# Optimization experiments

Measured on AMD Instinct MI355X. Metric: run time of the kernel, lower is better.

The kernel has to match this reference:

```python
import jax, jax.numpy as jnp
import numpy as np

B, C, U, V, H, W = 4, 64, 5, 5, 64, 64
MID = 64  # mid_dim defaults to dim


def setup_inputs() -> dict:
    key = jax.random.key(0)
    ks = jax.random.split(key, 13)
    s = 0.05
    inp = {"x": jax.random.normal(ks[0], (B, C, U, V, H, W), dtype=jnp.float32)}
    # body: Conv2d(dim->mid,1x1), SiLU, Conv2d(mid->dim,1x1)
    inp["w1"] = jax.random.normal(ks[1], (MID, C), dtype=jnp.float32) * s
    inp["b1"] = jax.random.normal(ks[2], (MID,), dtype=jnp.float32) * s
    inp["w2"] = jax.random.normal(ks[3], (C, MID), dtype=jnp.float32) * s
    inp["b2"] = jax.random.normal(ks[4], (C,), dtype=jnp.float32) * s
    # four fuse 1x1 convs (dim->dim)
    for i in range(4):
        inp[f"fw{i}"] = jax.random.normal(ks[5 + 2 * i], (C, C), dtype=jnp.float32) * s
        inp[f"fb{i}"] = jax.random.normal(ks[6 + 2 * i], (C,), dtype=jnp.float32) * s
    return inp


def _conv1x1(w, b, x):
    # x: (B,C,h,w); w: (O,C); 1x1 conv == channel matmul
    return jnp.einsum('oc,bchw->bohw', w, x) + b[None, :, None, None]


def reference(x, w1, b1, w2, b2, fw0, fb0, fw1, fb1, fw2, fb2, fw3, fb3):
    # Four 2-axis mean pools over the 6D tensor
    hw_m = x.mean(axis=(2, 3))   # (B,C,H,W)
    uv_m = x.mean(axis=(4, 5))   # (B,C,U,V)
    uh_m = x.mean(axis=(3, 5))   # (B,C,U,H)
    vw_m = x.mean(axis=(2, 4))   # (B,C,V,W)
    # Assemble padded buffer uvhw of shape (B,C,H+V,W+U)
    top = jnp.concatenate([hw_m, jnp.swapaxes(uh_m, -1, -2)], axis=-1)  # (B,C,H,W+U)
    bot = jnp.concatenate([vw_m, jnp.swapaxes(uv_m, -1, -2)], axis=-1)  # (B,C,V,W+U)
    uvhw = jnpp_concat = jnp.concatenate([top, bot], axis=-2)           # (B,C,H+V,W+U)
    # body: conv1x1 -> SiLU -> conv1x1
    uvhw = _conv1x1(w2, b2, jax.nn.silu(_conv1x1(w1, b1, uvhw)))
    # Split back into the four pooled maps
    hw = uvhw[..., :H, :W]
    vw = uvhw[..., H:, :W]
    uh = jnp.swapaxes(uvhw[..., :H, W:], -1, -2)  # (B,C,U,H)
    uv = jnp.swapaxes(uvhw[..., H:, W:], -1, -2)  # (B,C,U,V)
    # Per-branch fuse convs, then broadcast-gate x and sum
    hw = _conv1x1(fw0, fb0, hw).reshape(B, C, 1, 1, H, W)
    uv = _conv1x1(fw1, fb1, uv).reshape(B, C, U, V, 1, 1)
    uh = _conv1x1(fw2, fb2, uh).reshape(B, C, U, 1, H, 1)
    vw = _conv1x1(fw3, fb3, vw).reshape(B, C, 1, V, 1, W)
    return x * hw + x * uv + x * uh + x * vw
```

## Files before the change

### kernel.cpp

```cpp
#include <hip/hip_runtime.h>
#include <hip/hip_bf16.h>
#include <cstddef>

#define BB 4
#define CC 64
#define UU 5
#define VV 5
#define HH 64
#define WW 64

typedef float f4v __attribute__((ext_vector_type(4)));

__device__ __forceinline__ float rdlane(float v, int l) {
    return __uint_as_float((unsigned)__builtin_amdgcn_readlane((int)__float_as_uint(v), l));
}
__device__ __forceinline__ float rfl(float v) {
    return __uint_as_float((unsigned)__builtin_amdgcn_readfirstlane((int)__float_as_uint(v)));
}
__device__ __forceinline__ float sum4(float4 a) { return (a.x+a.y)+(a.z+a.w); }
__device__ __forceinline__ void nt_store4(float4 r, float4* p) {
    union { float4 s; f4v v; } u; u.s = r;
    __builtin_nontemporal_store(u.v, (f4v*)p);
}

__global__ __launch_bounds__(1024) void k1_means(const float* __restrict__ x,
        float* __restrict__ m_hw, float* __restrict__ R,
        float* __restrict__ vw_part) {
    const int bc   = blockIdx.x;
    const int t    = threadIdx.x;
    const int wave = t >> 6;
    const int lane = t & 63;

    const float4* xt = (const float4*)x + (size_t)bc * 25600;

    __shared__ float smem[25*1024];

    float4 hw = make_float4(0.f,0.f,0.f,0.f);
    float4 vwacc[5];
    #pragma unroll
    for (int v = 0; v < 5; ++v) vwacc[v] = make_float4(0.f,0.f,0.f,0.f);

    #pragma unroll
    for (int k = 0; k < 25; ++k) {
        float4 q = xt[(size_t)k*1024 + t];
        hw.x += q.x; hw.y += q.y; hw.z += q.z; hw.w += q.w;
        const int v = k % 5;
        vwacc[v].x += q.x; vwacc[v].y += q.y;
        vwacc[v].z += q.z; vwacc[v].w += q.w;
        smem[k*1024 + t] = sum4(q);
    }

    float4 o;
    o.x = hw.x*(1.f/25.f); o.y = hw.y*(1.f/25.f);
    o.z = hw.z*(1.f/25.f); o.w = hw.w*(1.f/25.f);
    ((float4*)m_hw)[(size_t)bc*1024 + t] = o;

    __syncthreads();

    for (int task = t; task < 1600; task += 1024) {
        const int k = task >> 6, h = task & 63;
        const float* row = &smem[k*1024 + h*16];
        float s = 0.f;
        #pragma unroll
        for (int j = 0; j < 16; ++j) s += row[j];
        R[((size_t)bc*25 + k)*64 + h] = s;
    }
    __syncthreads();

    float4* vwbuf = (float4*)smem;
    #pragma unroll
    for (int v = 0; v < 5; ++v) {
        float4 s = vwacc[v];
        s.x += __shfl_xor(s.x, 16); s.y += __shfl_xor(s.y, 16);
        s.z += __shfl_xor(s.z, 16); s.w += __shfl_xor(s.w, 16);
        s.x += __shfl_xor(s.x, 32); s.y += __shfl_xor(s.y, 32);
        s.z += __shfl_xor(s.z, 32); s.w += __shfl_xor(s.w, 32);
        if (lane < 16) vwbuf[(wave*5 + v)*16 + lane] = s;
    }
    __syncthreads();

    if (t < 80) {
        const int v = t >> 4;
        float4 s = vwbuf[(0*5 + v)*16 + (t & 15)];
        #pragma unroll
        for (int w16 = 1; w16 < 16; ++w16) {
            float4 pp = vwbuf[(w16*5 + v)*16 + (t & 15)];
            s.x += pp.x; s.y += pp.y; s.z += pp.z; s.w += pp.w;
        }
        ((float4*)vw_part)[(size_t)bc*80 + t] = s;
    }
}

#define LOADROW(dst, src)                                              \
    { _Pragma("unroll")                                                \
      for (int q = 0; q < 16; ++q) {                                   \
          float4 t4 = ((const float4*)(src))[lane*16 + q];             \
          dst[4*q+0] = t4.x; dst[4*q+1] = t4.y;                        \
          dst[4*q+2] = t4.z; dst[4*q+3] = t4.w;                        \
      } }

#define DOT64(res, wr, src)                                            \
    float res;                                                         \
    { float _a0=0.f,_a1=0.f,_a2=0.f,_a3=0.f;                           \
      _Pragma("unroll")                                                \
      for (int cc2 = 0; cc2 < 64; cc2 += 4) {                          \
          _a0 = fmaf(wr[cc2+0], rdlane(src, cc2+0), _a0);              \
          _a1 = fmaf(wr[cc2+1], rdlane(src, cc2+1), _a1);              \
          _a2 = fmaf(wr[cc2+2], rdlane(src, cc2+2), _a2);              \
          _a3 = fmaf(wr[cc2+3], rdlane(src, cc2+3), _a3);              \
      }                                                                \
      res = (_a0 + _a1) + (_a2 + _a3); }

#define MLP_CORE(VIN, OUTEXPR)                                         \
    {                                                                  \
        float v = (VIN);                                               \
        DOT64(d1, w1r, v);                                             \
        float acc1 = d1 + b1v;                                         \
        float ya = acc1 / (1.f + __expf(-acc1));                       \
        DOT64(d2, w2r, ya);                                            \
        float acc2 = d2 + b2v;                                         \
        DOT64(d3, fr, acc2);                                           \
        OUTEXPR = d3 + fbv;                                            \
    }

__global__ __launch_bounds__(64, 1) void k2_mlp(
        const float* __restrict__ m_hw, const float* __restrict__ R,
        const float* __restrict__ vw_part,
        const float* __restrict__ w1, const float* __restrict__ b1,
        const float* __restrict__ w2, const float* __restrict__ b2,
        const float* __restrict__ fw0, const float* __restrict__ fb0,
        const float* __restrict__ fw1, const float* __restrict__ fb1,
        const float* __restrict__ fw2, const float* __restrict__ fb2,
        const float* __restrict__ fw3, const float* __restrict__ fb3,
        float* __restrict__ mod_hw, float* __restrict__ mod_uh,
        float* __restrict__ mod_vw, float* __restrict__ mod_uv) {
    const int blk  = blockIdx.x;
    const int row  = blk / 3;
    const int chnk = blk % 3;
    const int b    = row / 69;
    const int i    = row % 69;
    const int lane = threadIdx.x & 63;

    const int j0 = chnk * 23;
    const int j1 = min(69, j0 + 23);
    const bool top = (i < 64);

    const float* fwA = top ? fw0 : fw3;
    const float* fbA = top ? fb0 : fb3;
    const float* fwB = top ? fw2 : fw1;
    const float* fbB = top ? fb2 : fb1;

    float w1r[64], w2r[64], fr[64];
    LOADROW(w1r, w1);
    LOADROW(w2r, w2);
    const float b1v = b1[lane];
    const float b2v = b2[lane];

    const int b64c = b * CC + lane;
    const int cbl  = b64c;

    const int jm = min(j1, 64);
    if (j0 < jm) {
        LOADROW(fr, fwA);
        const float fbv = fbA[lane];
        if (top) {
            const float* src = m_hw + (size_t)b64c*4096 + i*64;
            float* sp = mod_hw + ((size_t)cbl*64 + i)*64;
            for (int j = j0; j < jm; ++j)
                MLP_CORE(src[j], sp[j])
        } else {
            const float* pv = vw_part + (size_t)b64c*320 + (i-64)*64;
            float* sp = mod_vw + (size_t)cbl*320 + (i-64)*64;
            for (int j = j0; j < jm; ++j)
                MLP_CORE(pv[j] * (1.f/320.f), sp[j])
        }
    }
    if (j1 > 64) {
        LOADROW(fr, fwB);
        const float fbv = fbB[lane];
        const int jb = max(j0, 64);
        if (top) {
            float* sp = mod_uh + (size_t)cbl*320 + i;
            for (int j = jb; j < j1; ++j) {
                const int u = j - 64;
                const float* Rp = R + ((size_t)b64c*25 + u*5)*64 + i;
                float vin = (Rp[0] + Rp[64] + Rp[128] + Rp[192] + Rp[256])
                            * (1.f/320.f);
                MLP_CORE(vin, sp[(size_t)u*64])
            }
        } else {
            float* sp = mod_uv + (size_t)cbl*25 + (i-64);
            for (int j = jb; j < j1; ++j) {
                const int u = j - 64;
                const float4* Rp4 = (const float4*)(R
                    + ((size_t)b64c*25 + u*5 + (i-64))*64);
                float4 a = make_float4(0.f,0.f,0.f,0.f);
                #pragma unroll
                for (int k = 0; k < 16; ++k) {
                    float4 pp = Rp4[k];
                    a.x += pp.x; a.y += pp.y; a.z += pp.z; a.w += pp.w;
                }
                MLP_CORE(sum4(a) * (1.f/4096.f), sp[(size_t)u*5])
            }
        }
    }
}

__global__ __launch_bounds__(256, 4) void k3_apply(
        const float* __restrict__ x,
        const float* __restrict__ mod_hw, const float* __restrict__ mod_uh,
        const float* __restrict__ mod_vw, const float* __restrict__ mod_uv,
        float* __restrict__ out) {
    const int blk  = blockIdx.x;
    const int bc   = blk >> 2;
    const int qt   = blk & 3;
    const int t    = threadIdx.x;
    const int base = qt*256 + t;
    const int h    = base >> 4;

    float4 mh = ((const float4*)(mod_hw + (size_t)bc * 4096))[base];
    float uh[5];
    #pragma unroll
    for (int u = 0; u < 5; ++u) uh[u] = mod_uh[(size_t)bc*320 + u*64 + h];
    float4 vw[5];
    #pragma unroll
    for (int v = 0; v < 5; ++v)
        vw[v] = ((const float4*)(mod_vw + (size_t)bc*320 + v*64))[t & 15];
    float uv[25];
    #pragma unroll
    for (int k = 0; k < 25; ++k)
        uv[k] = rfl(mod_uv[(size_t)bc*25 + k]);

    const float4* x4 = (const float4*)(x + (size_t)bc * (UU*VV*HH*WW));
    float4* o4 = (float4*)(out + (size_t)bc * (UU*VV*HH*WW));

    #pragma unroll
    for (int u = 0; u < 5; ++u) {
        #pragma unroll
        for (int v = 0; v < 5; ++v) {
            const int idx = (u*5 + v)*1024 + base;
            float4 xv = x4[idx];
            const float s = uh[u] + uv[u*5 + v];
            float4 r;
            r.x = xv.x * (mh.x + vw[v].x + s);
            r.y = xv.y * (mh.y + vw[v].y + s);
            r.z = xv.z * (mh.z + vw[v].z + s);
            r.w = xv.w * (mh.w + vw[v].w + s);
            nt_store4(r, &o4[idx]);
        }
    }
}

extern "C" void kernel_launch(void* const* d_in, const int* in_sizes, int n_in,
                              void* d_out, int out_size, void* d_ws, size_t ws_size,
                              hipStream_t stream) {
    const float* x   = (const float*)d_in[0];
    const float* w1  = (const float*)d_in[1];
    const float* b1  = (const float*)d_in[2];
    const float* w2  = (const float*)d_in[3];
    const float* b2  = (const float*)d_in[4];
    const float* fw0 = (const float*)d_in[5];
    const float* fb0 = (const float*)d_in[6];
    const float* fw1 = (const float*)d_in[7];
    const float* fb1 = (const float*)d_in[8];
    const float* fw2 = (const float*)d_in[9];
    const float* fb2 = (const float*)d_in[10];
    const float* fw3 = (const float*)d_in[11];
    const float* fb3 = (const float*)d_in[12];

    float* ws = (float*)d_ws;
    float* mod_hw = ws;
    float* mod_uh = mod_hw + 1048576;
    float* mod_vw = mod_uh + 81920;
    float* mod_uv = mod_vw + 81920;

    float* m_hw    = (float*)d_out;
    float* Rbuf    = m_hw + 1048576;
    float* vw_part = Rbuf + 409600;

    k1_means<<<BB*CC, 1024, 0, stream>>>(x, m_hw, Rbuf, vw_part);
    k2_mlp<<<BB*69*3, 64, 0, stream>>>(m_hw, Rbuf, vw_part, w1, b1, w2, b2,
                                       fw0, fb0, fw1, fb1, fw2, fb2, fw3, fb3,
                                       mod_hw, mod_uh, mod_vw, mod_uv);
    k3_apply<<<BB*CC*4, 256, 0, stream>>>(x, mod_hw, mod_uh, mod_vw, mod_uv,
                                          (float*)d_out);
}
```

Measured before the change: 90.99 us.

## Split means kernel into four 256-thread blocks per channel with register-batched loads

The pooling kernel now launches four 256-thread blocks per (b,c) slice instead of one 1024-thread block, each covering a quarter of the H rows. All 25 float4 loads are issued up front into registers, and shared memory shrinks fourfold, which should improve occupancy and memory-level parallelism. The vw partial sums are now written per quarter-block, and the MLP kernel reduces the four partials itself, adding a few extra loads there.

```diff
diff --git a/kernel.cpp b/kernel.cpp
--- a/kernel.cpp
+++ b/kernel.cpp
@@ -23,47 +23,54 @@
     __builtin_nontemporal_store(u.v, (f4v*)p);
 }
 
-__global__ __launch_bounds__(1024) void k1_means(const float* __restrict__ x,
+__global__ __launch_bounds__(256) void k1_means(const float* __restrict__ x,
         float* __restrict__ m_hw, float* __restrict__ R,
         float* __restrict__ vw_part) {
-    const int bc   = blockIdx.x;
+    const int bid = blockIdx.x;
+    const int bc  = bid >> 2;
+    const int qt  = bid & 3;
     const int t    = threadIdx.x;
+    const int p    = qt*256 + t;
     const int wave = t >> 6;
     const int lane = t & 63;
 
-    const float4* xt = (const float4*)x + (size_t)bc * 25600;
-
-    __shared__ float smem[25*1024];
+    const float4* xt = (const float4*)x + (size_t)bc * 25600 + p;
+
+    __shared__ float smem[25*256];
+
+    float4 q[25];
+    #pragma unroll
+    for (int k = 0; k < 25; ++k)
+        q[k] = xt[(size_t)k*1024];
 
     float4 hw = make_float4(0.f,0.f,0.f,0.f);
     float4 vwacc[5];
     #pragma unroll
     for (int v = 0; v < 5; ++v) vwacc[v] = make_float4(0.f,0.f,0.f,0.f);
-
     #pragma unroll
     for (int k = 0; k < 25; ++k) {
-        float4 q = xt[(size_t)k*1024 + t];
-        hw.x += q.x; hw.y += q.y; hw.z += q.z; hw.w += q.w;
+        hw.x += q[k].x; hw.y += q[k].y; hw.z += q[k].z; hw.w += q[k].w;
         const int v = k % 5;
-        vwacc[v].x += q.x; vwacc[v].y += q.y;
-        vwacc[v].z += q.z; vwacc[v].w += q.w;
-        smem[k*1024 + t] = sum4(q);
+        vwacc[v].x += q[k].x; vwacc[v].y += q[k].y;
+        vwacc[v].z += q[k].z; vwacc[v].w += q[k].w;
+        smem[k*256 + t] = sum4(q[k]);
     }
 
     float4 o;
     o.x = hw.x*(1.f/25.f); o.y = hw.y*(1.f/25.f);
     o.z = hw.z*(1.f/25.f); o.w = hw.w*(1.f/25.f);
-    ((float4*)m_hw)[(size_t)bc*1024 + t] = o;
+    ((float4*)m_hw)[(size_t)bc*1024 + p] = o;
 
     __syncthreads();
 
-    for (int task = t; task < 1600; task += 1024) {
-        const int k = task >> 6, h = task & 63;
-        const float* row = &smem[k*1024 + h*16];
+    for (int task = t; task < 400; task += 256) {
+        const int k    = task >> 4;
+        const int hloc = task & 15;
+        const float* row = &smem[k*256 + hloc*16];
         float s = 0.f;
         #pragma unroll
         for (int j = 0; j < 16; ++j) s += row[j];
-        R[((size_t)bc*25 + k)*64 + h] = s;
+        R[((size_t)bc*25 + k)*64 + qt*16 + hloc] = s;
     }
     __syncthreads();
 
@@ -83,11 +90,11 @@
         const int v = t >> 4;
         float4 s = vwbuf[(0*5 + v)*16 + (t & 15)];
         #pragma unroll
-        for (int w16 = 1; w16 < 16; ++w16) {
-            float4 pp = vwbuf[(w16*5 + v)*16 + (t & 15)];
+        for (int w4 = 1; w4 < 4; ++w4) {
+            float4 pp = vwbuf[(w4*5 + v)*16 + (t & 15)];
             s.x += pp.x; s.y += pp.y; s.z += pp.z; s.w += pp.w;
         }
-        ((float4*)vw_part)[(size_t)bc*80 + t] = s;
+        ((float4*)vw_part)[(size_t)bid*80 + t] = s;
     }
 }
 
@@ -169,10 +176,13 @@
             for (int j = j0; j < jm; ++j)
                 MLP_CORE(src[j], sp[j])
         } else {
-            const float* pv = vw_part + (size_t)b64c*320 + (i-64)*64;
+            const float* pv = vw_part + (size_t)b64c*4*320 + (i-64)*64;
             float* sp = mod_vw + (size_t)cbl*320 + (i-64)*64;
-            for (int j = j0; j < jm; ++j)
-                MLP_CORE(pv[j] * (1.f/320.f), sp[j])
+            for (int j = j0; j < jm; ++j) {
+                float vin = ((pv[j] + pv[320 + j]) + (pv[640 + j] + pv[960 + j]))
+                            * (1.f/320.f);
+                MLP_CORE(vin, sp[j])
+            }
         }
     }
     if (j1 > 64) {
@@ -278,7 +288,7 @@
     float* Rbuf    = m_hw + 1048576;
     float* vw_part = Rbuf + 409600;
 
-    k1_means<<<BB*CC, 1024, 0, stream>>>(x, m_hw, Rbuf, vw_part);
+    k1_means<<<BB*CC*4, 256, 0, stream>>>(x, m_hw, Rbuf, vw_part);
     k2_mlp<<<BB*69*3, 64, 0, stream>>>(m_hw, Rbuf, vw_part, w1, b1, w2, b2,
                                        fw0, fb0, fw1, fb1, fw2, fb2, fw3, fb3,
                                        mod_hw, mod_uh, mod_vw, mod_uv);
```

Measured after the change: 91.39 us. No clear change (+0.4%).
